# Performance work log

Measured on AMD Instinct MI355X. Metric: run time of the kernel, lower is better.

## Reference

```python
import jax, jax.numpy as jnp
import numpy as np

DIM = 512
NUM_HEADS = 16
HEAD_DIM = DIM // NUM_HEADS
RES = (32, 32)
SEQ_SCALE = float(np.log(RES[0] * RES[1]))  # seq_length_scale buffer
TABLE = (2 * RES[0] - 1) * (2 * RES[1] - 1)  # 3969
EPS = 1e-12


def setup_inputs() -> dict:
    key = jax.random.key(0)
    ks = jax.random.split(key, 12)
    B, N, C = 8, RES[0] * RES[1], DIM
    s = 0.02
    return {
        "x": jax.random.normal(ks[0], (B, N, C), dtype=jnp.float32),
        "_h": RES[0],
        "_w": RES[1],
        "relative_pos_index": jax.random.randint(ks[1], (N, N), 0, TABLE, dtype=jnp.int32),
        "relative_coords_table": jax.random.uniform(ks[2], (TABLE, 2), dtype=jnp.float32, minval=-1.0, maxval=1.0),
        "qkv_w": jax.random.normal(ks[3], (3 * C, C), dtype=jnp.float32) * s,
        "qkv_b": jnp.zeros((3 * C,), dtype=jnp.float32),
        "proj_w": jax.random.normal(ks[4], (C, C), dtype=jnp.float32) * s,
        "proj_b": jnp.zeros((C,), dtype=jnp.float32),
        "temperature": jnp.full((NUM_HEADS, 1, 1), float(np.log(np.expm1(1.0 / 0.24))), dtype=jnp.float32),
        "query_embedding": jax.random.normal(ks[5], (NUM_HEADS, 1, HEAD_DIM), dtype=jnp.float32) * s,
        "cpb_fc1_w": jax.random.normal(ks[6], (512, 2), dtype=jnp.float32) * s,
        "cpb_fc1_b": jnp.zeros((512,), dtype=jnp.float32),
        "cpb_fc2_w": jax.random.normal(ks[7], (NUM_HEADS, 512), dtype=jnp.float32) * s,
        "cpb_fc2_b": jnp.zeros((NUM_HEADS,), dtype=jnp.float32),
    }


def _l2norm(t):
    # F.normalize(t, dim=-1): x / max(||x||, eps)
    n = jnp.sqrt(jnp.sum(t * t, axis=-1, keepdims=True))
    return t / jnp.maximum(n, EPS)


def reference(x, _h, _w, relative_pos_index, relative_coords_table,
              qkv_w, qkv_b, proj_w, proj_b, temperature, query_embedding,
              cpb_fc1_w, cpb_fc1_b, cpb_fc2_w, cpb_fc2_b):
    B, N, C = x.shape
    H, hd = NUM_HEADS, HEAD_DIM
    # qkv projection -> [B, N, 3H, hd] -> [B, 3H, N, hd]
    qkv = (x @ qkv_w.T + qkv_b).reshape(B, N, 3 * H, hd).transpose(0, 2, 1, 3)
    q, k, v = jnp.split(qkv, 3, axis=1)  # each [B, H, N, hd]
    # CPB MLP relative bias: [T,2] -> [T,H] -> gather -> [H,N,N]
    t = jax.nn.relu(relative_coords_table @ cpb_fc1_w.T + cpb_fc1_b) @ cpb_fc2_w.T + cpb_fc2_b
    rel_bias = t[relative_pos_index].transpose(2, 0, 1)  # [H, N, N]
    # cosine attention with learned softplus temperature and query embedding
    scale = jax.nn.softplus(temperature) * SEQ_SCALE  # [H,1,1]
    qn = (_l2norm(q) + query_embedding[None]) * scale[None]
    kn = _l2norm(k)
    attn = jnp.einsum('bhnd,bhmd->bhnm', qn, kn) + rel_bias[None]
    attn = jax.nn.softmax(attn, axis=-1)
    out = jnp.einsum('bhnm,bhmd->bhnd', attn, v)  # [B,H,N,hd]
    out = out.transpose(0, 2, 1, 3).reshape(B, N, C)
    return out @ proj_w.T + proj_b
```

## Files before the change

### kernel.cpp

```cpp
#include <hip/hip_runtime.h>
#include <cstdint>
#include <cstddef>

typedef _Float16 f16;
typedef _Float16 f16x4 __attribute__((ext_vector_type(4)));
typedef _Float16 f16x8 __attribute__((ext_vector_type(8)));
typedef float f32x4 __attribute__((ext_vector_type(4)));

#define MFMA32(a,b,c) __builtin_amdgcn_mfma_f32_16x16x32_f16((a),(b),(c),0,0,0)
#define MFMA16(a,b,c) __builtin_amdgcn_mfma_f32_16x16x16f16((a),(b),(c),0,0,0)

__device__ __forceinline__ float fexp2(float x) {
#if __has_builtin(__builtin_amdgcn_exp2f)
  return __builtin_amdgcn_exp2f(x);
#else
  return __expf(x * 0.69314718055994531f);
#endif
}

__device__ __forceinline__ void gload_lds16(const f16* g, f16* l) {
  __builtin_amdgcn_global_load_lds(
      (const __attribute__((address_space(1))) unsigned int*)g,
      (__attribute__((address_space(3))) unsigned int*)l, 16, 0, 0);
}

static constexpr size_t OFF_TCPB = 0;
static constexpr size_t OFF_BIAS = 262144;
static constexpr size_t OFF_XHI  = OFF_BIAS + 33554432;
static constexpr size_t OFF_XLO  = OFF_XHI + 8388608;
static constexpr size_t OFF_WHI  = OFF_XLO + 8388608;
static constexpr size_t OFF_WLO  = OFF_WHI + 1572864;
static constexpr size_t OFF_PW   = OFF_WLO + 1572864;
static constexpr size_t OFF_QHI  = OFF_PW  + 524288;
static constexpr size_t OFF_QLO  = OFF_QHI + 8388608;
static constexpr size_t OFF_KHI  = OFF_QLO + 8388608;
static constexpr size_t OFF_KLO  = OFF_KHI + 8388608;
static constexpr size_t OFF_VT   = OFF_KLO + 8388608;
static constexpr size_t OFF_AO   = OFF_VT  + 8388608;

__global__ __launch_bounds__(256) void k_convert(
    const float* __restrict__ x, const float* __restrict__ qw, const float* __restrict__ pwf,
    f16* __restrict__ xhi, f16* __restrict__ xlo,
    f16* __restrict__ whi, f16* __restrict__ pw)
{
  int i = blockIdx.x * 256 + threadIdx.x;
  const float4* src; f16* dh; f16* dl; int j;
  if (i < 1048576)      { j = i;           src = (const float4*)x;   dh = xhi; dl = xlo; }
  else if (i < 1245184) { j = i - 1048576; src = (const float4*)qw;  dh = whi; dl = nullptr; }
  else                  { j = i - 1245184; src = (const float4*)pwf; dh = pw;  dl = nullptr; }
  float4 v = src[j];
  f16x4 h;
  h[0] = (f16)v.x; h[1] = (f16)v.y; h[2] = (f16)v.z; h[3] = (f16)v.w;
  ((f16x4*)dh)[j] = h;
  if (dl) {
    f16x4 l;
    l[0] = (f16)(v.x - (float)h[0]); l[1] = (f16)(v.y - (float)h[1]);
    l[2] = (f16)(v.z - (float)h[2]); l[3] = (f16)(v.w - (float)h[3]);
    ((f16x4*)dl)[j] = l;
  }
}

__global__ __launch_bounds__(256) void k_cpb(
    const float* __restrict__ table, const float* __restrict__ w1, const float* __restrict__ b1,
    const float* __restrict__ w2, const float* __restrict__ b2, float* __restrict__ t_out)
{
  const int r = blockIdx.x * 4 + (threadIdx.x >> 6);
  const int lane = threadIdx.x & 63;
  if (r >= 3969) return;
  const float c0 = table[2*r], c1 = table[2*r+1];
  const int j0 = lane * 8;
  float h[8];
#pragma unroll
  for (int jj = 0; jj < 8; jj++) {
    int j = j0 + jj;
    float v = c0 * w1[2*j] + c1 * w1[2*j+1] + b1[j];
    h[jj] = v > 0.0f ? v : 0.0f;
  }
  float acc[16];
#pragma unroll
  for (int o = 0; o < 16; o++) {
    const float4* wp = (const float4*)(w2 + o*512 + j0);
    float4 a = wp[0], bb = wp[1];
    acc[o] = a.x*h[0] + a.y*h[1] + a.z*h[2] + a.w*h[3]
           + bb.x*h[4] + bb.y*h[5] + bb.z*h[6] + bb.w*h[7];
  }
#pragma unroll
  for (int o = 0; o < 16; o++) {
    float v = acc[o];
    for (int s = 1; s < 64; s <<= 1) v += __shfl_xor(v, s, 64);
    acc[o] = v;
  }
  if (lane == 0) {
#pragma unroll
    for (int o = 0; o < 16; o++)
      t_out[r*16 + o] = (acc[o] + b2[o]) * 1.4426950408889634f;
  }
}

__global__ __launch_bounds__(256) void k_bias(
    const int* __restrict__ idx, const float* __restrict__ t_cpb, f16* __restrict__ bias_t)
{
  int g = blockIdx.x * 256 + threadIdx.x;
  int n = g & 1023, m4 = g >> 10;
  int4 I = *(const int4*)(idx + (size_t)n*1024 + m4*4);
  int ids[4] = {I.x, I.y, I.z, I.w};
  const float4* T = (const float4*)t_cpb;
#pragma unroll
  for (int half = 0; half < 2; half++) {
    float4 R[4][2];
#pragma unroll
    for (int k = 0; k < 4; k++) {
      R[k][0] = T[ids[k]*4 + half*2];
      R[k][1] = T[ids[k]*4 + half*2 + 1];
    }
#pragma unroll
    for (int hh = 0; hh < 8; hh++) {
      int h = half*8 + hh;
      f16x4 o;
#pragma unroll
      for (int k = 0; k < 4; k++)
        o[k] = (f16)(((const float*)&R[k][hh >> 2])[hh & 3]);
      *(f16x4*)(bias_t + (((size_t)h*256 + m4)*1024 + n)*4) = o;
    }
  }
}

__global__ __launch_bounds__(256) void k_qkv(
    const f16* __restrict__ xhi, const f16* __restrict__ xlo,
    const f16* __restrict__ whi,
    const float* __restrict__ qkvb, const float* __restrict__ temp, const float* __restrict__ qe,
    f16* __restrict__ qh_o, f16* __restrict__ kh_o, f16* __restrict__ vt_o)
{
  __shared__ __align__(16) f16 Ah[8][64][8];
  __shared__ __align__(16) f16 Al[8][64][8];
  __shared__ __align__(16) f16 Bh[8][64][8];
  const int tid = threadIdx.x, lane = tid & 63, w = tid >> 6;
  const int rsel = lane & 15, ksel = lane >> 4;
  const int bx = blockIdx.x & 63, by = blockIdx.x >> 6;
  const int m0 = bx << 7, n0 = by << 7;
  const bool SPLIT = (by < 8);

  const size_t aoff = (size_t)(m0 + w*32 + rsel)*512 + ksel*8;
  const size_t boff = (size_t)(n0 + w*32 + rsel)*512 + ksel*8;
  const f16 *gA0 = xhi + aoff,  *gA1 = gA0 + 16*512;
  const f16 *gAl0 = xlo + aoff, *gAl1 = gAl0 + 16*512;
  const f16 *gB0 = whi + boff,  *gB1 = gB0 + 16*512;
  f16 *lA0 = &Ah[2*w][0][0],  *lA1 = &Ah[2*w+1][0][0];
  f16 *lAl0 = &Al[2*w][0][0], *lAl1 = &Al[2*w+1][0][0];
  f16 *lB0 = &Bh[2*w][0][0],  *lB1 = &Bh[2*w+1][0][0];

  const f32x4 zero = {0.f, 0.f, 0.f, 0.f};
  f32x4 acc[4][4];
#pragma unroll
  for (int mt = 0; mt < 4; mt++)
#pragma unroll
    for (int nt = 0; nt < 4; nt++) acc[mt][nt] = zero;

  const int mb4 = (w & 1) * 4, nb4 = (w >> 1) * 4;
  for (int k0 = 0; k0 < 512; k0 += 32) {
    __syncthreads();
    gload_lds16(gA0 + k0, lA0);
    gload_lds16(gA1 + k0, lA1);
    gload_lds16(gB0 + k0, lB0);
    gload_lds16(gB1 + k0, lB1);
    if (SPLIT) {
      gload_lds16(gAl0 + k0, lAl0);
      gload_lds16(gAl1 + k0, lAl1);
    }
    __syncthreads();
    f16x8 bhf[4];
#pragma unroll
    for (int nt = 0; nt < 4; nt++) bhf[nt] = ((const f16x8*)&Bh[nb4+nt][0][0])[lane];
    if (SPLIT) {
#pragma unroll
      for (int mt = 0; mt < 4; mt++) {
        f16x8 ah = ((const f16x8*)&Ah[mb4+mt][0][0])[lane];
        f16x8 al = ((const f16x8*)&Al[mb4+mt][0][0])[lane];
#pragma unroll
        for (int nt = 0; nt < 4; nt++) {
          acc[mt][nt] = MFMA32(al, bhf[nt], acc[mt][nt]);
          acc[mt][nt] = MFMA32(ah, bhf[nt], acc[mt][nt]);
        }
      }
    } else {
#pragma unroll
      for (int mt = 0; mt < 4; mt++) {
        f16x8 ah = ((const f16x8*)&Ah[mb4+mt][0][0])[lane];
#pragma unroll
        for (int nt = 0; nt < 4; nt++)
          acc[mt][nt] = MFMA32(ah, bhf[nt], acc[mt][nt]);
      }
    }
  }

  const int mbase = m0 + (w & 1)*64, nbase = n0 + (w >> 1)*64;
  float bc[4];
#pragma unroll
  for (int nt = 0; nt < 4; nt++) bc[nt] = qkvb[nbase + nt*16 + rsel];
#pragma unroll
  for (int mt = 0; mt < 4; mt++)
#pragma unroll
    for (int nt = 0; nt < 4; nt++)
#pragma unroll
      for (int r = 0; r < 4; r++) acc[mt][nt][r] += bc[nt];

  if (by < 8) {
    const bool ISQ = (by < 4);
#pragma unroll
    for (int pair = 0; pair < 2; pair++) {
      const int h = ((nbase - (ISQ ? 0 : 512)) >> 5) + pair;
      float sc = 0.f, qe0 = 0.f, qe1 = 0.f;
      if (ISQ) {
        sc  = log1pf(__expf(temp[h])) * 10.0f;
        qe0 = qe[h*32 + rsel];
        qe1 = qe[h*32 + 16 + rsel];
      }
      f16* dh = ISQ ? qh_o : kh_o;
#pragma unroll
      for (int mt = 0; mt < 4; mt++) {
        float ss[4];
#pragma unroll
        for (int r = 0; r < 4; r++) {
          float a = acc[mt][2*pair][r], b = acc[mt][2*pair+1][r];
          ss[r] = a*a + b*b;
        }
        for (int s = 1; s < 16; s <<= 1) {
#pragma unroll
          for (int r = 0; r < 4; r++) ss[r] += __shfl_xor(ss[r], s, 64);
        }
#pragma unroll
        for (int r = 0; r < 4; r++) {
          float rn = 1.0f / fmaxf(sqrtf(ss[r]), 1e-12f);
          int m = mbase + mt*16 + ksel*4 + r;
          int b_ = m >> 10, p = m & 1023;
          size_t base = ((size_t)(b_*16 + h)*1024 + p)*32;
          float v0 = acc[mt][2*pair][r] * rn;
          float v1 = acc[mt][2*pair+1][r] * rn;
          if (ISQ) { v0 = (v0 + qe0) * sc; v1 = (v1 + qe1) * sc; }
          dh[base + rsel]      = (f16)v0;
          dh[base + 16 + rsel] = (f16)v1;
        }
      }
    }
  } else {
#pragma unroll
    for (int mt = 0; mt < 4; mt++) {
      int m = mbase + mt*16 + ksel*4;
      int b_ = m >> 10, p = m & 1023;
#pragma unroll
      for (int nt = 0; nt < 4; nt++) {
        int n = nbase + nt*16 + rsel;
        int g = (n - 1024) >> 5, d = n & 31;
        f16x4 pk;
#pragma unroll
        for (int r = 0; r < 4; r++) pk[r] = (f16)acc[mt][nt][r];
        *(f16x4*)(vt_o + ((size_t)(b_*16 + g)*32 + d)*1024 + p) = pk;
      }
    }
  }
}

__global__ __launch_bounds__(256, 4) void k_attn(
    const f16* __restrict__ qhi, const f16* __restrict__ khi, const f16* __restrict__ vt,
    const f16* __restrict__ bias_t, f16* __restrict__ ao)
{
  __shared__ __align__(16) f16 OT[4][32][36];
  __shared__ __align__(16) float2 ML[4][32];
  const int lane = threadIdx.x & 63, w = threadIdx.x >> 6;
  const int rsel = lane & 15, ksel = lane >> 4;
  const int bid = blockIdx.x;
  const int xcd = bid & 7;
  const int r1 = bid >> 3;
  const int qt = r1 & 31;
  const int r2 = r1 >> 5;
  const int hHi = r2 & 1, b = r2 >> 1;
  const int h = (hHi << 3) | xcd;
  const int bh = b*16 + h;
  const int q0 = qt*32;
  const int mstart = w*256;

  f16x8 Qh[2];
#pragma unroll
  for (int c = 0; c < 2; c++)
    Qh[c] = *(const f16x8*)(qhi + ((size_t)bh*1024 + q0 + c*16 + rsel)*32 + ksel*8);

  const char* kb = (const char*)(khi + (size_t)bh*32768);
  const char* vb = (const char*)(vt  + (size_t)bh*32768);
  const char* bbp = (const char*)(bias_t + (size_t)h*1048576);
  int kOff = ((mstart + rsel)*32 + ksel*8) * 2;
  int vOff = (rsel*1024 + mstart + ksel*4) * 2;
  int bOff = (((mstart >> 2) + ksel)*1024 + q0 + rsel) * 8;

  f32x4 O[2][2];
  float mi[2], li[2];
#pragma unroll
  for (int c = 0; c < 2; c++) {
    O[c][0] = (f32x4){0.f,0.f,0.f,0.f};
    O[c][1] = (f32x4){0.f,0.f,0.f,0.f};
    mi[c] = -3.0e38f; li[c] = 0.f;
  }

  for (int it = 0; it < 8; ++it) {
    f16x8 K0 = *(const f16x8*)(kb + kOff);
    f16x8 K1 = *(const f16x8*)(kb + kOff + 1024);
    f16x4 Va[2][2], Bb[2][2];
    Va[0][0] = *(const f16x4*)(vb + vOff);
    Va[1][0] = *(const f16x4*)(vb + vOff + 32);
    Va[0][1] = *(const f16x4*)(vb + vOff + 32768);
    Va[1][1] = *(const f16x4*)(vb + vOff + 32800);
    Bb[0][0] = *(const f16x4*)(bbp + bOff);
    Bb[0][1] = *(const f16x4*)(bbp + bOff + 128);
    Bb[1][0] = *(const f16x4*)(bbp + bOff + 32768);
    Bb[1][1] = *(const f16x4*)(bbp + bOff + 32896);
    kOff += 2048; vOff += 64; bOff += 65536;

    f32x4 St[2][2];
#pragma unroll
    for (int f = 0; f < 2; f++)
#pragma unroll
      for (int c = 0; c < 2; c++) {
        f32x4 Ci;
#pragma unroll
        for (int r = 0; r < 4; r++) Ci[r] = (float)Bb[f][c][r];
        St[f][c] = MFMA32(f ? K1 : K0, Qh[c], Ci);
      }

    f16x4 P16[2][2];
#pragma unroll
    for (int c = 0; c < 2; c++) {
      float cm = fmaxf(fmaxf(fmaxf(St[0][c][0], St[0][c][1]), fmaxf(St[0][c][2], St[0][c][3])),
                       fmaxf(fmaxf(St[1][c][0], St[1][c][1]), fmaxf(St[1][c][2], St[1][c][3])));
      cm = fmaxf(cm, __shfl_xor(cm, 16, 64));
      cm = fmaxf(cm, __shfl_xor(cm, 32, 64));
      bool upd = cm > mi[c];
      float mn = upd ? cm : mi[c];
      float rs = 0.f;
#pragma unroll
      for (int f = 0; f < 2; f++)
#pragma unroll
        for (int r = 0; r < 4; r++) {
          float p = fexp2(St[f][c][r] - mn);
          rs += p;
          P16[f][c][r] = (f16)p;
        }
      if (__ballot(upd)) {
        float alpha = fexp2(mi[c] - mn);
        mi[c] = mn;
        li[c] = li[c]*alpha + rs;
#pragma unroll
        for (int dt = 0; dt < 2; dt++)
#pragma unroll
          for (int r = 0; r < 4; r++) O[c][dt][r] *= alpha;
      } else {
        li[c] += rs;
      }
    }
#pragma unroll
    for (int c = 0; c < 2; c++)
#pragma unroll
      for (int dt = 0; dt < 2; dt++) {
        O[c][dt] = MFMA16(Va[0][dt], P16[0][c], O[c][dt]);
        O[c][dt] = MFMA16(Va[1][dt], P16[1][c], O[c][dt]);
      }
  }

#pragma unroll
  for (int c = 0; c < 2; c++) {
    li[c] += __shfl_xor(li[c], 16, 64);
    li[c] += __shfl_xor(li[c], 32, 64);
    float inv = 1.0f / li[c];
#pragma unroll
    for (int dt = 0; dt < 2; dt++)
#pragma unroll
      for (int r = 0; r < 4; r++)
        OT[w][c*16 + rsel][dt*16 + ksel*4 + r] = (f16)(O[c][dt][r] * inv);
    if (ksel == 0) ML[w][c*16 + rsel] = make_float2(mi[c], li[c]);
  }
  __syncthreads();

  {
    int t = threadIdx.x;
    int q = t >> 3, dg = t & 7;
    float2 m0_ = ML[0][q], m1_ = ML[1][q], m2_ = ML[2][q], m3_ = ML[3][q];
    float M = fmaxf(fmaxf(m0_.x, m1_.x), fmaxf(m2_.x, m3_.x));
    float w0 = m0_.y * fexp2(m0_.x - M);
    float w1 = m1_.y * fexp2(m1_.x - M);
    float w2 = m2_.y * fexp2(m2_.x - M);
    float w3 = m3_.y * fexp2(m3_.x - M);
    float inv = 1.0f / (w0 + w1 + w2 + w3);
    f16x4 p0 = *(const f16x4*)(&OT[0][q][dg*4]);
    f16x4 p1 = *(const f16x4*)(&OT[1][q][dg*4]);
    f16x4 p2 = *(const f16x4*)(&OT[2][q][dg*4]);
    f16x4 p3 = *(const f16x4*)(&OT[3][q][dg*4]);
    f16x4 o;
#pragma unroll
    for (int r = 0; r < 4; r++)
      o[r] = (f16)(((float)p0[r]*w0 + (float)p1[r]*w1 + (float)p2[r]*w2 + (float)p3[r]*w3) * inv);
    *(f16x4*)(ao + ((size_t)b*1024 + q0 + q)*512 + h*32 + dg*4) = o;
  }
}

__global__ __launch_bounds__(256) void k_proj(
    const f16* __restrict__ A, const f16* __restrict__ Bw,
    const float* __restrict__ pb, float* __restrict__ out)
{
  __shared__ __align__(16) f16 Ah[8][64][8];
  __shared__ __align__(16) f16 Bh[8][64][8];
  const int tid = threadIdx.x, lane = tid & 63, w = tid >> 6;
  const int rsel = lane & 15, ksel = lane >> 4;
  const int bx = blockIdx.x & 63, by = blockIdx.x >> 6;
  const int m0 = bx << 7, n0 = by << 7;
  const f16 *gA0 = A + (size_t)(m0 + w*32 + rsel)*512 + ksel*8,  *gA1 = gA0 + 16*512;
  const f16 *gB0 = Bw + (size_t)(n0 + w*32 + rsel)*512 + ksel*8, *gB1 = gB0 + 16*512;
  f16 *lA0 = &Ah[2*w][0][0], *lA1 = &Ah[2*w+1][0][0];
  f16 *lB0 = &Bh[2*w][0][0], *lB1 = &Bh[2*w+1][0][0];
  const f32x4 zero = {0.f, 0.f, 0.f, 0.f};
  f32x4 acc[4][4];
#pragma unroll
  for (int mt = 0; mt < 4; mt++)
#pragma unroll
    for (int nt = 0; nt < 4; nt++) acc[mt][nt] = zero;
  const int mb4 = (w & 1)*4, nb4 = (w >> 1)*4;
  for (int k0 = 0; k0 < 512; k0 += 32) {
    __syncthreads();
    gload_lds16(gA0 + k0, lA0);
    gload_lds16(gA1 + k0, lA1);
    gload_lds16(gB0 + k0, lB0);
    gload_lds16(gB1 + k0, lB1);
    __syncthreads();
    f16x8 bhf[4];
#pragma unroll
    for (int nt = 0; nt < 4; nt++) bhf[nt] = ((const f16x8*)&Bh[nb4+nt][0][0])[lane];
#pragma unroll
    for (int mt = 0; mt < 4; mt++) {
      f16x8 ah = ((const f16x8*)&Ah[mb4+mt][0][0])[lane];
#pragma unroll
      for (int nt = 0; nt < 4; nt++)
        acc[mt][nt] = MFMA32(ah, bhf[nt], acc[mt][nt]);
    }
  }
  const int mbase = m0 + (w & 1)*64, nbase = n0 + (w >> 1)*64;
  float bc[4];
#pragma unroll
  for (int nt = 0; nt < 4; nt++) bc[nt] = pb[nbase + nt*16 + rsel];
#pragma unroll
  for (int mt = 0; mt < 4; mt++)
#pragma unroll
    for (int nt = 0; nt < 4; nt++)
#pragma unroll
      for (int r = 0; r < 4; r++)
        out[(size_t)(mbase + mt*16 + ksel*4 + r)*512 + nbase + nt*16 + rsel] =
            acc[mt][nt][r] + bc[nt];
}

extern "C" void kernel_launch(void* const* d_in, const int* in_sizes, int n_in,
                              void* d_out, int out_size, void* d_ws, size_t ws_size,
                              hipStream_t stream) {
  const float* x    = (const float*)d_in[0];
  const int*   rpi  = (const int*)d_in[3];
  const float* rct  = (const float*)d_in[4];
  const float* qw   = (const float*)d_in[5];
  const float* qb   = (const float*)d_in[6];
  const float* pwf  = (const float*)d_in[7];
  const float* pbv  = (const float*)d_in[8];
  const float* temp = (const float*)d_in[9];
  const float* qe   = (const float*)d_in[10];
  const float* f1w  = (const float*)d_in[11];
  const float* f1b  = (const float*)d_in[12];
  const float* f2w  = (const float*)d_in[13];
  const float* f2b  = (const float*)d_in[14];

  char* ws = (char*)d_ws;
  float* t_cpb  = (float*)(ws + OFF_TCPB);
  f16* bias_t   = (f16*)(ws + OFF_BIAS);
  f16* xhi = (f16*)(ws + OFF_XHI);
  f16* xlo = (f16*)(ws + OFF_XLO);
  f16* whi = (f16*)(ws + OFF_WHI);
  f16* pw  = (f16*)(ws + OFF_PW);
  f16* qhi = (f16*)(ws + OFF_QHI);
  f16* khi = (f16*)(ws + OFF_KHI);
  f16* vt  = (f16*)(ws + OFF_VT);
  f16* ao  = (f16*)(ws + OFF_AO);

  k_convert<<<5120, 256, 0, stream>>>(x, qw, pwf, xhi, xlo, whi, pw);
  k_cpb<<<993, 256, 0, stream>>>(rct, f1w, f1b, f2w, f2b, t_cpb);
  k_bias<<<1024, 256, 0, stream>>>(rpi, t_cpb, bias_t);
  k_qkv<<<768, 256, 0, stream>>>(xhi, xlo, whi, qb, temp, qe, qhi, khi, vt);
  k_attn<<<4096, 256, 0, stream>>>(qhi, khi, vt, bias_t, ao);
  k_proj<<<256, 256, 0, stream>>>(ao, pw, pbv, (float*)d_out);
}
```

Measured before the change: 282.9 us.

## Replace online softmax max tracking with precomputed per-head logit upper bound

Adds a tiny kernel that computes a per-head static upper bound on attention logits from the CPB bias maximum, softplus temperature and query-embedding norm. The attention kernel then subtracts this fixed offset instead of tracking a running max, removing the shuffles, ballot and rescaling per tile. The cross-wave merge becomes simple sums in fp32 LDS. The trade-off is possible underflow or lost precision if actual logits lie far below the bound.

```diff
diff --git a/kernel.cpp b/kernel.cpp
--- a/kernel.cpp
+++ b/kernel.cpp
@@ -97,6 +97,30 @@
   }
 }
 
+__global__ __launch_bounds__(256) void k_bound(
+    const float* __restrict__ t_cpb, const float* __restrict__ temp,
+    const float* __restrict__ qe, float* __restrict__ offs)
+{
+  __shared__ float red[256];
+  int t = threadIdx.x;
+  int h = t & 15, seg = t >> 4;
+  float mx = -1e30f;
+  for (int r = seg; r < 3969; r += 16)
+    mx = fmaxf(mx, t_cpb[r*16 + h]);
+  red[t] = mx;
+  __syncthreads();
+  if (t < 16) {
+    float m = red[t];
+#pragma unroll
+    for (int s = 1; s < 16; s++) m = fmaxf(m, red[t + s*16]);
+    float ss = 0.f;
+#pragma unroll
+    for (int j = 0; j < 32; j++) { float v = qe[t*32 + j]; ss += v*v; }
+    float sc = log1pf(__expf(temp[t])) * 10.0f;
+    offs[t] = 18.0f - (sc * (1.0f + sqrtf(ss)) + m);
+  }
+}
+
 __global__ __launch_bounds__(256) void k_bias(
     const int* __restrict__ idx, const float* __restrict__ t_cpb, f16* __restrict__ bias_t)
 {
@@ -262,10 +286,11 @@
 
 __global__ __launch_bounds__(256, 4) void k_attn(
     const f16* __restrict__ qhi, const f16* __restrict__ khi, const f16* __restrict__ vt,
-    const f16* __restrict__ bias_t, f16* __restrict__ ao)
-{
-  __shared__ __align__(16) f16 OT[4][32][36];
-  __shared__ __align__(16) float2 ML[4][32];
+    const f16* __restrict__ bias_t, const float* __restrict__ offs_arr,
+    f16* __restrict__ ao)
+{
+  __shared__ __align__(16) float OT[4][32][36];
+  __shared__ float ML[4][32];
   const int lane = threadIdx.x & 63, w = threadIdx.x >> 6;
   const int rsel = lane & 15, ksel = lane >> 4;
   const int bid = blockIdx.x;
@@ -278,6 +303,7 @@
   const int bh = b*16 + h;
   const int q0 = qt*32;
   const int mstart = w*256;
+  const float offs = offs_arr[h];
 
   f16x8 Qh[2];
 #pragma unroll
@@ -292,13 +318,9 @@
   int bOff = (((mstart >> 2) + ksel)*1024 + q0 + rsel) * 8;
 
   f32x4 O[2][2];
-  float mi[2], li[2];
-#pragma unroll
-  for (int c = 0; c < 2; c++) {
-    O[c][0] = (f32x4){0.f,0.f,0.f,0.f};
-    O[c][1] = (f32x4){0.f,0.f,0.f,0.f};
-    mi[c] = -3.0e38f; li[c] = 0.f;
-  }
+  float li[2] = {0.f, 0.f};
+  O[0][0] = (f32x4){0.f,0.f,0.f,0.f}; O[0][1] = O[0][0];
+  O[1][0] = O[0][0]; O[1][1] = O[0][0];
 
   for (int it = 0; it < 8; ++it) {
     f16x8 K0 = *(const f16x8*)(kb + kOff);
@@ -314,47 +336,24 @@
     Bb[1][1] = *(const f16x4*)(bbp + bOff + 32896);
     kOff += 2048; vOff += 64; bOff += 65536;
 
-    f32x4 St[2][2];
+    f16x4 P16[2][2];
 #pragma unroll
     for (int f = 0; f < 2; f++)
 #pragma unroll
       for (int c = 0; c < 2; c++) {
         f32x4 Ci;
 #pragma unroll
-        for (int r = 0; r < 4; r++) Ci[r] = (float)Bb[f][c][r];
-        St[f][c] = MFMA32(f ? K1 : K0, Qh[c], Ci);
-      }
-
-    f16x4 P16[2][2];
-#pragma unroll
-    for (int c = 0; c < 2; c++) {
-      float cm = fmaxf(fmaxf(fmaxf(St[0][c][0], St[0][c][1]), fmaxf(St[0][c][2], St[0][c][3])),
-                       fmaxf(fmaxf(St[1][c][0], St[1][c][1]), fmaxf(St[1][c][2], St[1][c][3])));
-      cm = fmaxf(cm, __shfl_xor(cm, 16, 64));
-      cm = fmaxf(cm, __shfl_xor(cm, 32, 64));
-      bool upd = cm > mi[c];
-      float mn = upd ? cm : mi[c];
-      float rs = 0.f;
-#pragma unroll
-      for (int f = 0; f < 2; f++)
+        for (int r = 0; r < 4; r++) Ci[r] = (float)Bb[f][c][r] + offs;
+        f32x4 St = MFMA32(f ? K1 : K0, Qh[c], Ci);
+        float rs = 0.f;
 #pragma unroll
         for (int r = 0; r < 4; r++) {
-          float p = fexp2(St[f][c][r] - mn);
+          float p = fexp2(St[r]);
           rs += p;
           P16[f][c][r] = (f16)p;
         }
-      if (__ballot(upd)) {
-        float alpha = fexp2(mi[c] - mn);
-        mi[c] = mn;
-        li[c] = li[c]*alpha + rs;
-#pragma unroll
-        for (int dt = 0; dt < 2; dt++)
-#pragma unroll
-          for (int r = 0; r < 4; r++) O[c][dt][r] *= alpha;
-      } else {
         li[c] += rs;
       }
-    }
 #pragma unroll
     for (int c = 0; c < 2; c++)
 #pragma unroll
@@ -368,34 +367,26 @@
   for (int c = 0; c < 2; c++) {
     li[c] += __shfl_xor(li[c], 16, 64);
     li[c] += __shfl_xor(li[c], 32, 64);
-    float inv = 1.0f / li[c];
 #pragma unroll
     for (int dt = 0; dt < 2; dt++)
 #pragma unroll
       for (int r = 0; r < 4; r++)
-        OT[w][c*16 + rsel][dt*16 + ksel*4 + r] = (f16)(O[c][dt][r] * inv);
-    if (ksel == 0) ML[w][c*16 + rsel] = make_float2(mi[c], li[c]);
+        OT[w][c*16 + rsel][dt*16 + ksel*4 + r] = O[c][dt][r];
+    if (ksel == 0) ML[w][c*16 + rsel] = li[c];
   }
   __syncthreads();
 
   {
     int t = threadIdx.x;
     int q = t >> 3, dg = t & 7;
-    float2 m0_ = ML[0][q], m1_ = ML[1][q], m2_ = ML[2][q], m3_ = ML[3][q];
-    float M = fmaxf(fmaxf(m0_.x, m1_.x), fmaxf(m2_.x, m3_.x));
-    float w0 = m0_.y * fexp2(m0_.x - M);
-    float w1 = m1_.y * fexp2(m1_.x - M);
-    float w2 = m2_.y * fexp2(m2_.x - M);
-    float w3 = m3_.y * fexp2(m3_.x - M);
-    float inv = 1.0f / (w0 + w1 + w2 + w3);
-    f16x4 p0 = *(const f16x4*)(&OT[0][q][dg*4]);
-    f16x4 p1 = *(const f16x4*)(&OT[1][q][dg*4]);
-    f16x4 p2 = *(const f16x4*)(&OT[2][q][dg*4]);
-    f16x4 p3 = *(const f16x4*)(&OT[3][q][dg*4]);
+    float L = ML[0][q] + ML[1][q] + ML[2][q] + ML[3][q];
+    float inv = 1.0f / L;
     f16x4 o;
 #pragma unroll
-    for (int r = 0; r < 4; r++)
-      o[r] = (f16)(((float)p0[r]*w0 + (float)p1[r]*w1 + (float)p2[r]*w2 + (float)p3[r]*w3) * inv);
+    for (int r = 0; r < 4; r++) {
+      float s = OT[0][q][dg*4+r] + OT[1][q][dg*4+r] + OT[2][q][dg*4+r] + OT[3][q][dg*4+r];
+      o[r] = (f16)(s * inv);
+    }
     *(f16x4*)(ao + ((size_t)b*1024 + q0 + q)*512 + h*32 + dg*4) = o;
   }
 }
@@ -476,6 +467,7 @@
   f16* xhi = (f16*)(ws + OFF_XHI);
   f16* xlo = (f16*)(ws + OFF_XLO);
   f16* whi = (f16*)(ws + OFF_WHI);
+  float* offs = (float*)(ws + OFF_WLO);
   f16* pw  = (f16*)(ws + OFF_PW);
   f16* qhi = (f16*)(ws + OFF_QHI);
   f16* khi = (f16*)(ws + OFF_KHI);
@@ -484,8 +476,9 @@
 
   k_convert<<<5120, 256, 0, stream>>>(x, qw, pwf, xhi, xlo, whi, pw);
   k_cpb<<<993, 256, 0, stream>>>(rct, f1w, f1b, f2w, f2b, t_cpb);
+  k_bound<<<1, 256, 0, stream>>>(t_cpb, temp, qe, offs);
   k_bias<<<1024, 256, 0, stream>>>(rpi, t_cpb, bias_t);
   k_qkv<<<768, 256, 0, stream>>>(xhi, xlo, whi, qb, temp, qe, qhi, khi, vt);
-  k_attn<<<4096, 256, 0, stream>>>(qhi, khi, vt, bias_t, ao);
+  k_attn<<<4096, 256, 0, stream>>>(qhi, khi, vt, bias_t, offs, ao);
   k_proj<<<256, 256, 0, stream>>>(ao, pw, pbv, (float*)d_out);
 }
```

Result: slower. 323.2 us (+14.2%).
